# Performance work log

Measured on AMD Instinct MI355X. Metric: run time of the kernel, lower is better.

Reference implementation:

```python
import jax, jax.numpy as jnp
import numpy as np

TOPK = 13
ALPHA = 1.0
BETA = 6.0
EPS = 1e-9


def setup_inputs() -> dict:
    key = jax.random.key(0)
    ks = jax.random.split(key, 8)
    B, A, C, M = 32, 8400, 80, 64
    IMG = 640.0
    pred_scores = jax.random.uniform(ks[0], (B, A, C), jnp.float32)  # sigmoid-like scores in [0,1]
    anchor_points = jax.random.uniform(ks[1], (A, 2), jnp.float32, 0.0, IMG)
    off = jax.random.uniform(ks[2], (B, A, 4), jnp.float32, 4.0, 64.0)
    # valid x1y1x2y2 predicted boxes around anchor centers
    pred_bboxes = jnp.concatenate([anchor_points[None] - off[..., :2],
                                   anchor_points[None] + off[..., 2:]], axis=-1)
    gt_labels = jax.random.randint(ks[3], (B, M, 1), 0, C, jnp.int32)
    cxy = jax.random.uniform(ks[4], (B, M, 2), jnp.float32, 20.0, IMG - 20.0)
    wh = jax.random.uniform(ks[5], (B, M, 2), jnp.float32, 8.0, 200.0)
    gt_bboxes = jnp.concatenate([jnp.clip(cxy - 0.5 * wh, 0.0, IMG),
                                 jnp.clip(cxy + 0.5 * wh, 0.0, IMG)], axis=-1)
    nvalid = jax.random.randint(ks[6], (B, 1), 8, M + 1)
    pad_gt_mask = (jnp.arange(M)[None, :] < nvalid).astype(jnp.float32)[..., None]  # [B,M,1] prefix mask
    return {"pred_scores": pred_scores, "pred_bboxes": pred_bboxes,
            "anchor_points": anchor_points, "gt_labels": gt_labels,
            "gt_bboxes": gt_bboxes, "pad_gt_mask": pad_gt_mask, "bg_index": 80}


def reference(pred_scores, pred_bboxes, anchor_points, gt_labels, gt_bboxes, pad_gt_mask, bg_index):
    B, A, C = pred_scores.shape
    M = gt_bboxes.shape[1]

    # ---- pairwise IoU: gt [B,M,1,4] vs pred [B,1,A,4] -> [B,M,A] ----
    b1 = gt_bboxes[:, :, None, :]
    b2 = pred_bboxes[:, None, :, :]
    x1y1 = jnp.maximum(b1[..., :2], b2[..., :2])
    x2y2 = jnp.minimum(b1[..., 2:], b2[..., 2:])
    overlap = jnp.prod(jnp.clip(x2y2 - x1y1, 0.0, None), axis=-1)
    area1 = jnp.prod(jnp.clip(b1[..., 2:] - b1[..., :2], 0.0, None), axis=-1)
    area2 = jnp.prod(jnp.clip(b2[..., 2:] - b2[..., :2], 0.0, None), axis=-1)
    ious = overlap / (area1 + area2 - overlap + EPS)  # [B,M,A]

    # ---- classification score of each anchor at each GT's label -> [B,M,A] ----
    scores_t = jnp.transpose(pred_scores, (0, 2, 1))  # [B,C,A]
    bbox_cls_scores = jnp.take_along_axis(scores_t, gt_labels, axis=1)  # idx [B,M,1] -> [B,M,A]

    align = (bbox_cls_scores ** ALPHA) * (ious ** BETA)  # alignment metric [B,M,A]

    # ---- anchors-inside-gt mask [B,M,A] ----
    px = anchor_points[None, None, :, 0]
    py = anchor_points[None, None, :, 1]
    xmin = gt_bboxes[:, :, None, 0]; ymin = gt_bboxes[:, :, None, 1]
    xmax = gt_bboxes[:, :, None, 2]; ymax = gt_bboxes[:, :, None, 3]
    d = jnp.minimum(jnp.minimum(px - xmin, py - ymin), jnp.minimum(xmax - px, ymax - py))
    is_in_gts = (d > EPS).astype(align.dtype)

    # ---- top-k gating along anchors ----
    metrics = align * is_in_gts
    _, topk_idxs = jax.lax.top_k(metrics, TOPK)  # [B,M,TOPK]
    bi = jnp.arange(B)[:, None, None]
    mi = jnp.arange(M)[None, :, None]
    is_in_topk = jnp.zeros_like(metrics).at[bi, mi, topk_idxs].add(1.0)
    is_in_topk = is_in_topk * pad_gt_mask  # topk_mask = pad_gt_mask

    mask_positive = is_in_topk * is_in_gts * pad_gt_mask  # [B,M,A]
    mask_positive_sum = mask_positive.sum(axis=-2)  # [B,A]

    # ---- resolve anchors claimed by multiple GTs via max-IoU ----
    multi = (mask_positive_sum[:, None, :] > 1)  # [B,1,A] broadcasts over M
    max_iou_idx = jnp.argmax(ious, axis=-2)  # [B,A]
    is_max_iou = (jnp.arange(M)[None, :, None] == max_iou_idx[:, None, :]).astype(ious.dtype)
    mask_positive = jnp.where(multi, is_max_iou, mask_positive)
    mask_positive_sum = mask_positive.sum(axis=-2)

    # ---- assemble assignments ----
    assigned_gt_index = jnp.argmax(mask_positive, axis=-2)  # [B,A]
    assigned_labels = jnp.take_along_axis(gt_labels[..., 0], assigned_gt_index, axis=1)  # [B,A]
    assigned_labels = jnp.where(mask_positive_sum > 0, assigned_labels, bg_index)
    assigned_bboxes = jnp.take_along_axis(gt_bboxes, assigned_gt_index[..., None], axis=1)  # [B,A,4]

    one_hot = jax.nn.one_hot(assigned_labels, C + 1, dtype=align.dtype)
    keep = jnp.array([i for i in range(C + 1) if i != bg_index], dtype=jnp.int32)
    assigned_scores = one_hot[..., keep]  # [B,A,C]

    # ---- rescale alignment metrics into soft targets ----
    am = align * mask_positive
    max_metrics = am.max(axis=-1, keepdims=True)  # [B,M,1]
    max_ious = (ious * mask_positive).max(axis=-1, keepdims=True)
    am = am / (max_metrics + EPS) * max_ious
    assigned_scores = assigned_scores * am.max(axis=-2)[..., None]

    return assigned_labels, assigned_bboxes, assigned_scores
```

## Files before the change

### kernel.cpp

```cpp
#include <hip/hip_runtime.h>
#include <stdint.h>

#define BB 32
#define AA 8400
#define CC 80
#define MM 64
#define KTOP 13
#define FEPS 1e-9f
#define CAND_CAP 1024
#define CNT_STRIDE 16
#define PLIST_CAP (BB * MM * KTOP)

typedef unsigned long long u64;

__device__ __forceinline__ float iou_fn(float gx1, float gy1, float gx2, float gy2,
                                        float px1, float py1, float px2, float py2) {
    float ix1 = fmaxf(gx1, px1), iy1 = fmaxf(gy1, py1);
    float ix2 = fminf(gx2, px2), iy2 = fminf(gy2, py2);
    float ov = fmaxf(ix2 - ix1, 0.0f) * fmaxf(iy2 - iy1, 0.0f);
    float a1 = fmaxf(gx2 - gx1, 0.0f) * fmaxf(gy2 - gy1, 0.0f);
    float a2 = fmaxf(px2 - px1, 0.0f) * fmaxf(py2 - py1, 0.0f);
    return ov / (a1 + a2 - ov + FEPS);
}

__global__ __launch_bounds__(256) void pairgen_kernel(
    const float* __restrict__ pred_scores, const float* __restrict__ pred_bboxes,
    const float* __restrict__ anchors, const int* __restrict__ gt_labels,
    const float* __restrict__ gt_bboxes, const float* __restrict__ pad_mask,
    int* __restrict__ cnt, u64* __restrict__ cand, u64* __restrict__ mask64)
{
    __shared__ float4 gtb_s[MM];
    __shared__ int    gtl_s[MM];
    __shared__ u64    valid_s;
    int b = blockIdx.y;
    int t = threadIdx.x;
    if (t < MM) {
        gtb_s[t] = ((const float4*)gt_bboxes)[b * MM + t];
        gtl_s[t] = gt_labels[b * MM + t];
        bool v = pad_mask[b * MM + t] != 0.0f;
        u64 bal = __ballot(v);
        if (t == 0) valid_s = bal;
    }
    __syncthreads();
    int a = blockIdx.x * 256 + t;
    if (a >= AA) return;
    mask64[(size_t)b * AA + a] = 0ull;
    float2 xy = *(const float2*)(anchors + a * 2);
    float4 p = ((const float4*)pred_bboxes)[(size_t)b * AA + a];
    const float4* gg = (const float4*)gt_bboxes + b * MM;
    u64 mask = 0;
    #pragma unroll 8
    for (int m = 0; m < MM; ++m) {
        float4 g = gg[m];
        float d = fminf(fminf(xy.x - g.x, xy.y - g.y), fminf(g.z - xy.x, g.w - xy.y));
        mask |= ((u64)(d > FEPS)) << m;
    }
    mask &= valid_s;
    if (!mask) return;
    float parea = (p.z - p.x) * (p.w - p.y);
    const float* psa = pred_scores + ((size_t)b * AA + a) * CC;
    unsigned ia = (unsigned)(AA - a);
    while (mask) {
        int m = __ffsll(mask) - 1;
        mask &= mask - 1;
        float4 g = gtb_s[m];
        float ix1 = fmaxf(g.x, p.x), iy1 = fmaxf(g.y, p.y);
        float ix2 = fminf(g.z, p.z), iy2 = fminf(g.w, p.w);
        float ov = fmaxf(ix2 - ix1, 0.0f) * fmaxf(iy2 - iy1, 0.0f);
        float garea = (g.z - g.x) * (g.w - g.y);
        float iou = ov / (garea + parea - ov + FEPS);
        float s = psa[gtl_s[m]];
        float i2 = iou * iou;
        float met = s * (i2 * i2 * i2);
        if (met > 0.0f) {
            int bm = b * MM + m;
            int slot = atomicAdd(&cnt[bm * CNT_STRIDE], 1);
            if (slot < CAND_CAP)
                cand[(size_t)bm * CAND_CAP + slot] =
                    ((u64)__float_as_uint(met) << 32) | ia;
        }
    }
}

__global__ __launch_bounds__(256) void select_scatter_kernel(
    const int* __restrict__ cnt, const u64* __restrict__ cand,
    u64* __restrict__ mask64)
{
    int bm = blockIdx.x;
    int n = min(cnt[bm * CNT_STRIDE], CAND_CAP);
    int rounds = min(n, KTOP);
    if (rounds == 0) return;
    int b = bm >> 6, m = bm & 63;
    int t = threadIdx.x;
    __shared__ u64 rv[2][4];
    u64 c[4];
    #pragma unroll
    for (int j = 0; j < 4; ++j) {
        int i = t + j * 256;
        c[j] = (i < n) ? cand[(size_t)bm * CAND_CAP + i] : 0;
    }
    int lane = t & 63, wv = t >> 6;
    for (int k = 0; k < rounds; ++k) {
        u64 bk = c[0];
        #pragma unroll
        for (int j = 1; j < 4; ++j) bk = (c[j] > bk) ? c[j] : bk;
        #pragma unroll
        for (int off = 32; off > 0; off >>= 1) {
            u64 ok = __shfl_xor(bk, off);
            bk = (ok > bk) ? ok : bk;
        }
        if (lane == 0) rv[k & 1][wv] = bk;
        __syncthreads();
        u64 wk = rv[k & 1][0];
        #pragma unroll
        for (int w = 1; w < 4; ++w) wk = (rv[k & 1][w] > wk) ? rv[k & 1][w] : wk;
        #pragma unroll
        for (int j = 0; j < 4; ++j) if (c[j] == wk) c[j] = 0;
        if (t == 0) {
            int a = AA - (int)(wk & 0xffffffffULL);
            atomicOr(&mask64[(size_t)b * AA + a], 1ull << m);
        }
    }
}

__global__ __launch_bounds__(256) void resolve_kernel(
    const float* __restrict__ pred_scores, const float* __restrict__ pred_bboxes,
    const int* __restrict__ gt_labels, const float* __restrict__ gt_bboxes,
    const int* __restrict__ bg_ptr,
    const u64* __restrict__ mask64,
    float* __restrict__ out_labels, float* __restrict__ out_bboxes,
    float* __restrict__ assigned_align,
    unsigned int* __restrict__ maxmet, unsigned int* __restrict__ maxiou,
    int* __restrict__ pcnt, int2* __restrict__ plist)
{
    __shared__ float4 gtb_s[MM];
    __shared__ int    gtl_s[MM];
    __shared__ int    lcnt, lbase;
    int b = blockIdx.y;
    int t = threadIdx.x;
    if (t == 0) lcnt = 0;
    if (t < MM) {
        gtb_s[t] = ((const float4*)gt_bboxes)[b * MM + t];
        gtl_s[t] = gt_labels[b * MM + t];
    }
    __syncthreads();
    int a = blockIdx.x * 256 + t;
    bool active = (a < AA);
    int mstar = -1, myslot = -1;
    size_t ga = 0;
    if (active) {
        ga = (size_t)b * AA + a;
        u64 mask = mask64[ga];
        int pc = __popcll(mask);
        float4 p = ((const float4*)pred_bboxes)[ga];
        if (pc == 1) {
            mstar = __ffsll(mask) - 1;
        } else if (pc > 1) {
            float best = -1.0f; int bi = 0;
            for (int m = 0; m < MM; ++m) {
                float4 g = gtb_s[m];
                float iou = iou_fn(g.x, g.y, g.z, g.w, p.x, p.y, p.z, p.w);
                if (iou > best) { best = iou; bi = m; }
            }
            mstar = bi;
        }
        int bidx = (mstar >= 0) ? mstar : 0;
        float4 g = gtb_s[bidx];
        ((float4*)out_bboxes)[ga] = g;
        out_labels[ga] = (mstar >= 0) ? (float)gtl_s[mstar] : (float)(*bg_ptr);
        if (mstar >= 0) {
            float iou = iou_fn(g.x, g.y, g.z, g.w, p.x, p.y, p.z, p.w);
            float s = pred_scores[ga * CC + gtl_s[mstar]];
            float i2 = iou * iou;
            float al = s * (i2 * i2 * i2);
            assigned_align[ga] = al;
            atomicMax(&maxmet[b * MM + mstar], __float_as_uint(al));
            atomicMax(&maxiou[b * MM + mstar], __float_as_uint(iou));
            myslot = atomicAdd(&lcnt, 1);
        }
    }
    __syncthreads();
    if (t == 0 && lcnt > 0) lbase = atomicAdd(pcnt, lcnt);
    __syncthreads();
    if (myslot >= 0) plist[lbase + myslot] = make_int2((int)ga, mstar);
}

__global__ __launch_bounds__(256) void fixup_kernel(
    const int* __restrict__ gt_labels,
    const int* __restrict__ pcnt, const int2* __restrict__ plist,
    const float* __restrict__ assigned_align,
    const unsigned int* __restrict__ maxmet, const unsigned int* __restrict__ maxiou,
    float* __restrict__ out_scores)
{
    int i = blockIdx.x * blockDim.x + threadIdx.x;
    if (i >= *pcnt) return;
    int2 e = plist[i];
    size_t ga = (size_t)e.x;
    int m = e.y;
    int b = (int)(ga / AA);
    int label = gt_labels[b * MM + m];
    float mm = __uint_as_float(maxmet[b * MM + m]);
    float mi = __uint_as_float(maxiou[b * MM + m]);
    float scale = assigned_align[ga] / (mm + FEPS) * mi;
    out_scores[ga * CC + label] = scale;
}

extern "C" void kernel_launch(void* const* d_in, const int* in_sizes, int n_in,
                              void* d_out, int out_size, void* d_ws, size_t ws_size,
                              hipStream_t stream) {
    const float* pred_scores = (const float*)d_in[0];
    const float* pred_bboxes = (const float*)d_in[1];
    const float* anchors     = (const float*)d_in[2];
    const int*   gt_labels   = (const int*)d_in[3];
    const float* gt_bboxes   = (const float*)d_in[4];
    const float* pad_mask    = (const float*)d_in[5];
    const int*   bg_ptr      = (const int*)d_in[6];

    char* ws = (char*)d_ws;
    size_t off = 0;
    int* cnt = (int*)(ws + off);
    off += (size_t)BB * MM * CNT_STRIDE * sizeof(int);
    unsigned int* maxmet = (unsigned int*)(ws + off);
    off += (size_t)BB * MM * sizeof(unsigned int);
    unsigned int* maxiou = (unsigned int*)(ws + off);
    off += (size_t)BB * MM * sizeof(unsigned int);
    int* pcnt = (int*)(ws + off);
    off += 16;
    size_t zero_bytes = off;
    u64* mask64 = (u64*)(ws + off);
    off += (size_t)BB * AA * sizeof(u64);
    u64* cand = (u64*)(ws + off);
    off += (size_t)BB * MM * CAND_CAP * sizeof(u64);
    float* assigned_align = (float*)(ws + off);
    off += (size_t)BB * AA * sizeof(float);
    int2* plist = (int2*)(ws + off);
    off += (size_t)PLIST_CAP * sizeof(int2);

    hipMemsetAsync(ws, 0, zero_bytes, stream);

    float* out = (float*)d_out;
    float* out_labels = out;
    float* out_bboxes = out + (size_t)BB * AA;
    float* out_scores = out + (size_t)BB * AA * 5;

    hipMemsetAsync(out_scores, 0, (size_t)BB * AA * CC * sizeof(float), stream);

    dim3 gridA((AA + 255) / 256, BB);
    pairgen_kernel<<<gridA, 256, 0, stream>>>(
        pred_scores, pred_bboxes, anchors, gt_labels, gt_bboxes, pad_mask,
        cnt, cand, mask64);

    select_scatter_kernel<<<BB * MM, 256, 0, stream>>>(cnt, cand, mask64);

    resolve_kernel<<<gridA, 256, 0, stream>>>(
        pred_scores, pred_bboxes, gt_labels, gt_bboxes, bg_ptr, mask64,
        out_labels, out_bboxes, assigned_align, maxmet, maxiou, pcnt, plist);

    fixup_kernel<<<(PLIST_CAP + 255) / 256, 256, 0, stream>>>(
        gt_labels, pcnt, plist, assigned_align, maxmet, maxiou, out_scores);
}
```

Before: 238.1 us.

## Fuse fixup into resolve via last-block pattern and shrink memset

Removes the separate fixup kernel launch. The last block to finish resolve_kernel, detected with an atomic done counter and threadfences, now does the score rescaling. The zeroing of maxmet, maxiou, pcnt and done moves into select_scatter_kernel, which shrinks the host memset. This saves one launch plus a small memset, but the whole fixup (up to about 26k entries) now runs serially in a single 256-thread block, which may be slower than the parallel kernel it replaces.

```diff
diff --git a/kernel.cpp b/kernel.cpp
--- a/kernel.cpp
+++ b/kernel.cpp
@@ -84,14 +84,21 @@
 
 __global__ __launch_bounds__(256) void select_scatter_kernel(
     const int* __restrict__ cnt, const u64* __restrict__ cand,
-    u64* __restrict__ mask64)
+    u64* __restrict__ mask64,
+    unsigned int* __restrict__ maxmet, unsigned int* __restrict__ maxiou,
+    int* __restrict__ pcnt, int* __restrict__ done)
 {
     int bm = blockIdx.x;
+    int t = threadIdx.x;
+    if (t == 0) {
+        maxmet[bm] = 0u;
+        maxiou[bm] = 0u;
+        if (bm == 0) { *pcnt = 0; *done = 0; }
+    }
     int n = min(cnt[bm * CNT_STRIDE], CAND_CAP);
     int rounds = min(n, KTOP);
     if (rounds == 0) return;
     int b = bm >> 6, m = bm & 63;
-    int t = threadIdx.x;
     __shared__ u64 rv[2][4];
     u64 c[4];
     #pragma unroll
@@ -129,13 +136,14 @@
     const int* __restrict__ bg_ptr,
     const u64* __restrict__ mask64,
     float* __restrict__ out_labels, float* __restrict__ out_bboxes,
+    float* __restrict__ out_scores,
     float* __restrict__ assigned_align,
     unsigned int* __restrict__ maxmet, unsigned int* __restrict__ maxiou,
-    int* __restrict__ pcnt, int2* __restrict__ plist)
+    int* __restrict__ pcnt, int2* __restrict__ plist, int* __restrict__ done)
 {
     __shared__ float4 gtb_s[MM];
     __shared__ int    gtl_s[MM];
-    __shared__ int    lcnt, lbase;
+    __shared__ int    lcnt, lbase, islast;
     int b = blockIdx.y;
     int t = threadIdx.x;
     if (t == 0) lcnt = 0;
@@ -183,26 +191,29 @@
     if (t == 0 && lcnt > 0) lbase = atomicAdd(pcnt, lcnt);
     __syncthreads();
     if (myslot >= 0) plist[lbase + myslot] = make_int2((int)ga, mstar);
-}
-
-__global__ __launch_bounds__(256) void fixup_kernel(
-    const int* __restrict__ gt_labels,
-    const int* __restrict__ pcnt, const int2* __restrict__ plist,
-    const float* __restrict__ assigned_align,
-    const unsigned int* __restrict__ maxmet, const unsigned int* __restrict__ maxiou,
-    float* __restrict__ out_scores)
-{
-    int i = blockIdx.x * blockDim.x + threadIdx.x;
-    if (i >= *pcnt) return;
-    int2 e = plist[i];
-    size_t ga = (size_t)e.x;
-    int m = e.y;
-    int b = (int)(ga / AA);
-    int label = gt_labels[b * MM + m];
-    float mm = __uint_as_float(maxmet[b * MM + m]);
-    float mi = __uint_as_float(maxiou[b * MM + m]);
-    float scale = assigned_align[ga] / (mm + FEPS) * mi;
-    out_scores[ga * CC + label] = scale;
+
+    __syncthreads();
+    __threadfence();
+    if (t == 0) {
+        int old = atomicAdd(done, 1);
+        islast = (old == (int)(gridDim.x * gridDim.y) - 1);
+    }
+    __syncthreads();
+    if (islast) {
+        __threadfence();
+        int n = atomicAdd(pcnt, 0);
+        for (int i = t; i < n; i += 256) {
+            int2 e = plist[i];
+            size_t pga = (size_t)e.x;
+            int m = e.y;
+            int pb = (int)(pga / AA);
+            int label = gt_labels[pb * MM + m];
+            float mm = __uint_as_float(maxmet[pb * MM + m]);
+            float mi = __uint_as_float(maxiou[pb * MM + m]);
+            out_scores[pga * CC + label] =
+                assigned_align[pga] / (mm + FEPS) * mi;
+        }
+    }
 }
 
 extern "C" void kernel_launch(void* const* d_in, const int* in_sizes, int n_in,
@@ -220,13 +231,15 @@
     size_t off = 0;
     int* cnt = (int*)(ws + off);
     off += (size_t)BB * MM * CNT_STRIDE * sizeof(int);
+    size_t zero_bytes = off;
     unsigned int* maxmet = (unsigned int*)(ws + off);
     off += (size_t)BB * MM * sizeof(unsigned int);
     unsigned int* maxiou = (unsigned int*)(ws + off);
     off += (size_t)BB * MM * sizeof(unsigned int);
     int* pcnt = (int*)(ws + off);
     off += 16;
-    size_t zero_bytes = off;
+    int* done = (int*)(ws + off);
+    off += 16;
     u64* mask64 = (u64*)(ws + off);
     off += (size_t)BB * AA * sizeof(u64);
     u64* cand = (u64*)(ws + off);
@@ -250,12 +263,11 @@
         pred_scores, pred_bboxes, anchors, gt_labels, gt_bboxes, pad_mask,
         cnt, cand, mask64);
 
-    select_scatter_kernel<<<BB * MM, 256, 0, stream>>>(cnt, cand, mask64);
+    select_scatter_kernel<<<BB * MM, 256, 0, stream>>>(
+        cnt, cand, mask64, maxmet, maxiou, pcnt, done);
 
     resolve_kernel<<<gridA, 256, 0, stream>>>(
         pred_scores, pred_bboxes, gt_labels, gt_bboxes, bg_ptr, mask64,
-        out_labels, out_bboxes, assigned_align, maxmet, maxiou, pcnt, plist);
-
-    fixup_kernel<<<(PLIST_CAP + 255) / 256, 256, 0, stream>>>(
-        gt_labels, pcnt, plist, assigned_align, maxmet, maxiou, out_scores);
-}
+        out_labels, out_bboxes, out_scores, assigned_align,
+        maxmet, maxiou, pcnt, plist, done);
+}
```

New measurement: 336.2 us. 1.41x slower.
